# Kernel tuning notes

Hardware: AMD Instinct MI355X
Metric: run time of the kernel (lower is better)

The kernel has to match this reference:

```python
import jax, jax.numpy as jnp
import numpy as np

N_NODES = 50000
N_EDGES = 400000
IN_DIM = 4
HID = 32
NCLASSES = 4
N_ITERS = 3


def setup_inputs() -> dict:
    key = jax.random.key(0)
    ks = jax.random.split(key, 8)

    def w(k, shape, fan_in):
        return (jax.random.normal(k, shape, dtype=jnp.float32) / np.sqrt(fan_in)).astype(jnp.float32)

    x = jax.random.normal(ks[0], (3, N_NODES, IN_DIM), dtype=jnp.float32)
    edge_index = jax.random.randint(ks[1], (3, 2, N_EDGES), 0, N_NODES, dtype=jnp.int64)
    hi = HID + IN_DIM  # 36: feats of m = cat([H, X])
    return {
        "x": x,
        "edge_index": edge_index,
        "in_W": w(ks[2], (3, IN_DIM, HID), IN_DIM),
        "in_b": jnp.zeros((3, HID), jnp.float32),
        "eW1": w(ks[3], (3, 2 * hi, HID), 2 * hi),
        "eb1": jnp.zeros((3, HID), jnp.float32),
        "eW2": w(ks[4], (3, HID, 1), HID),
        "eb2": jnp.zeros((3, 1), jnp.float32),
        "nW1": w(ks[5], (3, 3 * hi, HID), 3 * hi),
        "nb1": jnp.zeros((3, HID), jnp.float32),
        "nW2": w(ks[6], (3, HID, HID), HID),
        "nb2": jnp.zeros((3, HID), jnp.float32),
    }


def _forward(x, edge_index, in_W, in_b, eW1, eb1, eW2, eb2, nW1, nb1, nW2, nb2):
    n_nodes = x.shape[1]

    def edge_net(j, m, row, col):
        # B: [E, C, 2*(h+in)] -- detached in the original module
        B = jax.lax.stop_gradient(jnp.concatenate([m[col], m[row]], axis=-1))
        t = jnp.tanh(B @ eW1[j] + eb1[j])
        t = jnp.tanh(t @ eW2[j] + eb2[j])  # [E, C, 1]
        return jax.nn.softmax(t, axis=1)  # softmax over class dim

    def node_net(j, m, ea, row, col):
        mi = jax.ops.segment_sum(ea * m[row], col, num_segments=n_nodes)
        mo = jax.ops.segment_sum(ea * m[col], row, num_segments=n_nodes)
        M = jnp.concatenate([mi, mo, m], axis=-1)  # [N, C, 3*(h+in)]
        t = jnp.tanh(M @ nW1[j] + nb1[j])
        return jnp.tanh(t @ nW2[j] + nb2[j])  # [N, C, hid]

    rows = [edge_index[j, 0] for j in range(3)]
    cols = [edge_index[j, 1] for j in range(3)]
    # X: node feats repeated per class, [N, C, in]
    X = [jnp.broadcast_to(x[j][:, None, :], (n_nodes, NCLASSES, x.shape[-1])) for j in range(3)]
    H = [jnp.tanh(X[j] @ in_W[j] + in_b[j]) for j in range(3)]
    m = [jnp.concatenate([H[j], X[j]], axis=-1) for j in range(3)]

    for _ in range(N_ITERS):
        for j in range(3):
            ea = edge_net(j, m[j], rows[j], cols[j])
            H[j] = node_net(j, m[j], ea, rows[j], cols[j])
        m = [jnp.concatenate([H[j], X[j]], axis=-1) for j in range(3)]

    # classify_node=False: final edge-network pass per plane, squeeze -> [E, C]
    ret = [edge_net(j, m[j], rows[j], cols[j])[..., 0] for j in range(3)]
    return jnp.concatenate(ret, axis=0)  # [3*E, C]


def reference(x, edge_index, in_W, in_b, eW1, eb1, eW2, eb2, nW1, nb1, nW2, nb2):
    return _forward(x, edge_index, in_W, in_b, eW1, eb1, eW2, eb2, nW1, nb1, nW2, nb2)
```

## Files before the change

### kernel.cpp

```cpp
#include <hip/hip_runtime.h>
#include <hip/hip_fp16.h>

#define N_NODES 50000
#define N_EDGES 400000
#define NCLS 4
#define HID 32
#define HI 36
#define ROWS_P (N_NODES * NCLS)
#define PADCAP 672000
#define SLICES 8
#define BUCKS_PER_SLICE (N_NODES / SLICES)

__device__ __forceinline__ float fast_tanh(float x) {
    x = fminf(15.0f, fmaxf(-15.0f, x));
    float e = __expf(2.0f * x);
    float d = 1.0f + e;
    float r = __builtin_amdgcn_rcpf(d);
    r = r * (2.0f - d * r);
    return 1.0f - 2.0f * r;
}

union F4H8 { float4 f4; __half2 h2[4]; };

__global__ void k_init(const float* __restrict__ x, const float* __restrict__ W,
                       const float* __restrict__ b, float* __restrict__ m) {
    unsigned t = blockIdx.x * 256 + threadIdx.x;
    if (t >= N_NODES * HI) return;
    unsigned idx = t % HI;
    unsigned n   = t / HI;
    float x0 = x[n * 4 + 0], x1 = x[n * 4 + 1];
    float x2 = x[n * 4 + 2], x3 = x[n * 4 + 3];
    float val;
    if (idx < 32) {
        float a = b[idx];
        a += x0 * W[idx] + x1 * W[32 + idx] + x2 * W[64 + idx] + x3 * W[96 + idx];
        val = fast_tanh(a);
    } else {
        val = (idx == 32) ? x0 : (idx == 33) ? x1 : (idx == 34) ? x2 : x3;
    }
    float* dst = m + (size_t)n * (NCLS * HI) + idx;
    dst[0] = val; dst[HI] = val; dst[2 * HI] = val; dst[3 * HI] = val;
}

__global__ void k_pass1(const int* __restrict__ rowI, const int* __restrict__ colI,
                        int* __restrict__ inCnt, int* __restrict__ outCnt,
                        int* __restrict__ tmpLi) {
    unsigned e = blockIdx.x * 256 + threadIdx.x;
    if (e >= N_EDGES) return;
    int r = rowI[e], cn = colI[e];
    int liIn  = atomicAdd(&inCnt[cn], 1);
    int liOut = atomicAdd(&outCnt[r], 1);
    tmpLi[e] = liIn | (liOut << 16);
}

__global__ void k_scan(const int* __restrict__ inCnt, const int* __restrict__ outCnt,
                       int* __restrict__ inOffRaw, int* __restrict__ pinOff,
                       int* __restrict__ poutOff) {
    const int* cnt = (blockIdx.x == 2) ? outCnt : inCnt;
    int* off = (blockIdx.x == 0) ? inOffRaw : (blockIdx.x == 1) ? pinOff : poutOff;
    bool pad = blockIdx.x != 0;
    __shared__ int sh[16];
    __shared__ int carry;
    int tid = threadIdx.x;
    int lane = tid & 63, wid = tid >> 6;
    if (tid == 0) carry = 0;
    __syncthreads();
    for (int base = 0; base < N_NODES; base += 1024) {
        int i = base + tid;
        int v = (i < N_NODES) ? cnt[i] : 0;
        if (pad) v = (v + 7) & ~7;
        int val = v;
#pragma unroll
        for (int d = 1; d < 64; d <<= 1) {
            int t = __shfl_up(val, d, 64);
            if (lane >= d) val += t;
        }
        if (lane == 63) sh[wid] = val;
        __syncthreads();
        if (tid < 16) {
            int s = sh[tid];
#pragma unroll
            for (int d = 1; d < 16; d <<= 1) {
                int t = __shfl_up(s, d, 16);
                if (tid >= d) s += t;
            }
            sh[tid] = s;
        }
        __syncthreads();
        int waveOff = (wid == 0) ? 0 : sh[wid - 1];
        int incl = val + waveOff + carry;
        if (i < N_NODES) off[i] = incl - v;
        __syncthreads();
        if (tid == 1023) carry = incl;
        __syncthreads();
    }
    if (tid == 0) off[N_NODES] = carry;
}

__global__ void k_pass2(const int* __restrict__ rowI, const int* __restrict__ colI,
                        const int* __restrict__ tmpLi,
                        const int* __restrict__ inOffRaw, const int* __restrict__ pinOff,
                        const int* __restrict__ poutOff,
                        int4* __restrict__ edgeRec,
                        unsigned short* __restrict__ inPrt,
                        unsigned short* __restrict__ outPrt) {
    unsigned b = blockIdx.x;
    unsigned slice = b & (SLICES - 1);
    unsigned e = (b >> 3) * 256 + threadIdx.x;
    if (e >= N_EDGES) return;
    int r = rowI[e], cn = colI[e];
    int li = tmpLi[e];
    int liIn  = li & 0xFFFF;
    int liOut = (int)(((unsigned)li) >> 16);
    unsigned lo = slice * BUCKS_PER_SLICE;
    if ((unsigned)(cn - lo) < BUCKS_PER_SLICE) {
        int dense = inOffRaw[cn] + liIn;
        int piP   = pinOff[cn] + liIn;
        int poP   = poutOff[r] + liOut;
        edgeRec[dense] = make_int4(r | (cn << 16), piP, poP, (int)e);
        inPrt[piP] = (unsigned short)r;
    }
    if ((unsigned)(r - lo) < BUCKS_PER_SLICE) {
        int poP = poutOff[r] + liOut;
        outPrt[poP] = (unsigned short)cn;
    }
}


__global__ void k_gemm5(const float* __restrict__ m,
                        const float* __restrict__ eW1, const float* __restrict__ nW1,
                        __half* __restrict__ u, __half* __restrict__ v,
                        __half* __restrict__ p, __half* __restrict__ q,
                        __half* __restrict__ r) {
    constexpr int RPB = 32;
    __shared__ float sm[RPB * HI];
    unsigned tid = threadIdx.x;
    unsigned r0  = blockIdx.x * RPB;
    {
        const float4* gsrc = reinterpret_cast<const float4*>(m + (size_t)r0 * HI);
        float4* ldst = reinterpret_cast<float4*>(sm);
        for (unsigned i = tid; i < RPB * HI / 4; i += 320) ldst[i] = gsrc[i];
    }
    unsigned o = tid % 160, grp = tid / 160;
    unsigned sub = o >> 5, oo = o & 31;
    const float* W = (sub == 0) ? eW1 : (sub == 1) ? eW1 + 36 * 32 :
                     (sub == 2) ? nW1 : (sub == 3) ? nW1 + 36 * 32 : nW1 + 72 * 32;
    __half* dsth   = (sub == 0) ? u : (sub == 1) ? v : (sub == 2) ? p :
                     (sub == 3) ? q : r;
    float wcol[36];
#pragma unroll
    for (int k = 0; k < 36; ++k) wcol[k] = W[k * 32 + oo];
    __syncthreads();
#pragma unroll
    for (int i = 0; i < 16; ++i) {
        unsigned rloc = grp * 16 + i;
        const float4* mv4 = reinterpret_cast<const float4*>(sm + rloc * HI);
        float acc = 0.f;
#pragma unroll
        for (int t = 0; t < 9; ++t) {
            float4 mv = mv4[t];
            acc += mv.x * wcol[4 * t + 0];
            acc += mv.y * wcol[4 * t + 1];
            acc += mv.z * wcol[4 * t + 2];
            acc += mv.w * wcol[4 * t + 3];
        }
        dsth[(size_t)(r0 + rloc) * 32 + oo] = __float2half_rn(acc);
    }
}

__global__ void k_gemm2(const float* __restrict__ m, const float* __restrict__ W0,
                        const float* __restrict__ W1,
                        __half* __restrict__ o0, __half* __restrict__ o1) {
    constexpr int RPB = 32;
    __shared__ float sm[RPB * HI];
    unsigned tid = threadIdx.x;
    unsigned r0  = blockIdx.x * RPB;
    {
        const float4* gsrc = reinterpret_cast<const float4*>(m + (size_t)r0 * HI);
        float4* ldst = reinterpret_cast<float4*>(sm);
        for (unsigned i = tid; i < RPB * HI / 4; i += 256) ldst[i] = gsrc[i];
    }
    unsigned o = tid % 64, grp = tid / 64;
    unsigned sub = o >> 5, oo = o & 31;
    const float* W = sub ? W1 : W0;
    __half* dst    = sub ? o1 : o0;
    float wcol[36];
#pragma unroll
    for (int k = 0; k < 36; ++k) wcol[k] = W[k * 32 + oo];
    __syncthreads();
#pragma unroll
    for (int i = 0; i < 8; ++i) {
        unsigned rloc = grp * 8 + i;
        const float4* mv4 = reinterpret_cast<const float4*>(sm + rloc * HI);
        float acc = 0.f;
#pragma unroll
        for (int t = 0; t < 9; ++t) {
            float4 mv = mv4[t];
            acc += mv.x * wcol[4 * t + 0];
            acc += mv.y * wcol[4 * t + 1];
            acc += mv.z * wcol[4 * t + 2];
            acc += mv.w * wcol[4 * t + 3];
        }
        dst[(size_t)(r0 + rloc) * 32 + oo] = __float2half_rn(acc);
    }
}

template <bool FINAL>
__global__ void k_edge(const int4* __restrict__ edgeRec,
                       const __half* __restrict__ u, const __half* __restrict__ v,
                       const float* __restrict__ b1, const float* __restrict__ w2,
                       const float* __restrict__ b2,
                       __half* __restrict__ eaIn, __half* __restrict__ eaOut,
                       float* __restrict__ dst) {
    unsigned g   = blockIdx.x * 256 + threadIdx.x;
    unsigned c   = g & 3;
    unsigned idx = g >> 2;
    int4 rec = edgeRec[idx];
    unsigned rc  = (unsigned)rec.x;
    unsigned row = rc & 0xFFFFu, col = rc >> 16;
    const float4* u4 = reinterpret_cast<const float4*>(u + (col * 4 + c) * 32);
    const float4* v4 = reinterpret_cast<const float4*>(v + (row * 4 + c) * 32);
    float t2 = b2[0];
#pragma unroll
    for (int i = 0; i < 4; ++i) {
        F4H8 U, V; U.f4 = u4[i]; V.f4 = v4[i];
#pragma unroll
        for (int jj = 0; jj < 4; ++jj) {
            float2 uf = __half22float2(U.h2[jj]);
            float2 vf = __half22float2(V.h2[jj]);
            int o = i * 8 + jj * 2;
            t2 += fast_tanh(uf.x + vf.x + b1[o])     * w2[o];
            t2 += fast_tanh(uf.y + vf.y + b1[o + 1]) * w2[o + 1];
        }
    }
    float s  = fast_tanh(t2);
    float m1 = fmaxf(s, __shfl_xor(s, 1, 4));
    float mx = fmaxf(m1, __shfl_xor(m1, 2, 4));
    float ex = __expf(s - mx);
    float sm = ex + __shfl_xor(ex, 1, 4);
    sm = sm + __shfl_xor(sm, 2, 4);
    float val = ex / sm;
    if (FINAL) {
        dst[(unsigned)rec.w * 4 + c] = val;
    } else {
        __half hv = __float2half_rn(val);
        eaIn[(size_t)c * PADCAP + (unsigned)rec.y] = hv;
        eaOut[(size_t)c * PADCAP + (unsigned)rec.z] = hv;
    }
}

__global__ void __launch_bounds__(64, 4)
k_node(float* __restrict__ m, const __half* __restrict__ rbuf,
       const __half* __restrict__ p, const __half* __restrict__ q,
       const __half* __restrict__ eaInT, const __half* __restrict__ eaOutT,
       const int* __restrict__ pinOff, const int* __restrict__ poutOff,
       const unsigned short* __restrict__ inPrt,
       const unsigned short* __restrict__ outPrt,
       const float* __restrict__ nb1,
       const float* __restrict__ nW2, const float* __restrict__ nb2) {
    unsigned lane = threadIdx.x;
    unsigned c2 = lane >> 5, k = lane & 31;
    unsigned n = blockIdx.x;
    unsigned gOff0 = c2 * 32 + k;
    unsigned gOff1 = gOff0 + 64;

    float b1k = nb1[k];
    float h0 = __half2float(rbuf[((size_t)n * 4 + c2) * 32 + k]) + b1k;
    float h1 = __half2float(rbuf[((size_t)n * 4 + c2 + 2) * 32 + k]) + b1k;

    int bi0 = pinOff[n],  biE = pinOff[n + 1];
    int bo0 = poutOff[n], boE = poutOff[n + 1];
    __builtin_assume((bi0 & 7) == 0);
    __builtin_assume((bo0 & 7) == 0);

    auto accum = [&](const __half* __restrict__ base, uint4 prtv, uint4 e0v, uint4 e1v) {
        unsigned pr0 = prtv.x & 0xFFFFu, pr1 = prtv.x >> 16;
        unsigned pr2 = prtv.y & 0xFFFFu, pr3 = prtv.y >> 16;
        unsigned pr4 = prtv.z & 0xFFFFu, pr5 = prtv.z >> 16;
        unsigned pr6 = prtv.w & 0xFFFFu, pr7 = prtv.w >> 16;
        __half g0h[8], g1h[8];
        const __half* r0p = base + (size_t)pr0 * 128u; g0h[0] = r0p[gOff0]; g1h[0] = r0p[gOff1];
        const __half* r1p = base + (size_t)pr1 * 128u; g0h[1] = r1p[gOff0]; g1h[1] = r1p[gOff1];
        const __half* r2p = base + (size_t)pr2 * 128u; g0h[2] = r2p[gOff0]; g1h[2] = r2p[gOff1];
        const __half* r3p = base + (size_t)pr3 * 128u; g0h[3] = r3p[gOff0]; g1h[3] = r3p[gOff1];
        const __half* r4p = base + (size_t)pr4 * 128u; g0h[4] = r4p[gOff0]; g1h[4] = r4p[gOff1];
        const __half* r5p = base + (size_t)pr5 * 128u; g0h[5] = r5p[gOff0]; g1h[5] = r5p[gOff1];
        const __half* r6p = base + (size_t)pr6 * 128u; g0h[6] = r6p[gOff0]; g1h[6] = r6p[gOff1];
        const __half* r7p = base + (size_t)pr7 * 128u; g0h[7] = r7p[gOff0]; g1h[7] = r7p[gOff1];
        union { uint4 u4; __half2 h2[4]; } E0, E1;
        E0.u4 = e0v; E1.u4 = e1v;
#pragma unroll
        for (int ii = 0; ii < 4; ++ii) {
            float2 A0 = __half22float2(E0.h2[ii]);
            float2 A1 = __half22float2(E1.h2[ii]);
            h0 += A0.x * __half2float(g0h[2 * ii]) + A0.y * __half2float(g0h[2 * ii + 1]);
            h1 += A1.x * __half2float(g1h[2 * ii]) + A1.y * __half2float(g1h[2 * ii + 1]);
        }
    };

    uint4 oprt = {0, 0, 0, 0}, oe0 = {0, 0, 0, 0}, oe1 = {0, 0, 0, 0};
    if (bo0 < boE) {
        oprt = *(const uint4*)(outPrt + bo0);
        oe0  = *(const uint4*)(eaOutT + (size_t)c2 * PADCAP + bo0);
        oe1  = *(const uint4*)(eaOutT + (size_t)(c2 + 2) * PADCAP + bo0);
    }

    if (bi0 < biE) {
        uint4 cprt = *(const uint4*)(inPrt + bi0);
        uint4 ce0  = *(const uint4*)(eaInT + (size_t)c2 * PADCAP + bi0);
        uint4 ce1  = *(const uint4*)(eaInT + (size_t)(c2 + 2) * PADCAP + bi0);
        for (int b = bi0; b < biE; b += 8) {
            uint4 nprt = cprt, ne0 = ce0, ne1 = ce1;
            if (b + 8 < biE) {
                nprt = *(const uint4*)(inPrt + b + 8);
                ne0  = *(const uint4*)(eaInT + (size_t)c2 * PADCAP + b + 8);
                ne1  = *(const uint4*)(eaInT + (size_t)(c2 + 2) * PADCAP + b + 8);
            }
            accum(p, cprt, ce0, ce1);
            cprt = nprt; ce0 = ne0; ce1 = ne1;
        }
    }
    if (bo0 < boE) {
        uint4 cprt = oprt, ce0 = oe0, ce1 = oe1;
        for (int b = bo0; b < boE; b += 8) {
            uint4 nprt = cprt, ne0 = ce0, ne1 = ce1;
            if (b + 8 < boE) {
                nprt = *(const uint4*)(outPrt + b + 8);
                ne0  = *(const uint4*)(eaOutT + (size_t)c2 * PADCAP + b + 8);
                ne1  = *(const uint4*)(eaOutT + (size_t)(c2 + 2) * PADCAP + b + 8);
            }
            accum(q, cprt, ce0, ce1);
            cprt = nprt; ce0 = ne0; ce1 = ne1;
        }
    }

    float t0 = fast_tanh(h0);
    float t1 = fast_tanh(h1);
    float hh0 = nb2[k], hh1 = hh0;
#pragma unroll
    for (int kk = 0; kk < 32; ++kk) {
        float w = nW2[kk * 32 + k];
        float s0 = __shfl(t0, (int)(c2 * 32 + kk), 64);
        float s1 = __shfl(t1, (int)(c2 * 32 + kk), 64);
        hh0 += s0 * w;
        hh1 += s1 * w;
    }
    m[((size_t)n * 4 + c2) * HI + k]     = fast_tanh(hh0);
    m[((size_t)n * 4 + c2 + 2) * HI + k] = fast_tanh(hh1);
}

extern "C" void kernel_launch(void* const* d_in, const int* in_sizes, int n_in,
                              void* d_out, int out_size, void* d_ws, size_t ws_size,
                              hipStream_t stream) {
    const float* x   = (const float*)d_in[0];
    const int*   ei  = (const int*)d_in[1];
    const float* inW = (const float*)d_in[2];
    const float* inb = (const float*)d_in[3];
    const float* eW1 = (const float*)d_in[4];
    const float* eb1 = (const float*)d_in[5];
    const float* eW2 = (const float*)d_in[6];
    const float* eb2 = (const float*)d_in[7];
    const float* nW1 = (const float*)d_in[8];
    const float* nb1 = (const float*)d_in[9];
    const float* nW2 = (const float*)d_in[10];
    const float* nb2 = (const float*)d_in[11];
    float* out = (float*)d_out;

    float*  m     = (float*)d_ws;
    __half* u     = (__half*)(m + (size_t)ROWS_P * HI);
    __half* v     = u + (size_t)ROWS_P * 32;
    __half* p     = v + (size_t)ROWS_P * 32;
    __half* q     = p + (size_t)ROWS_P * 32;
    __half* rbuf  = q + (size_t)ROWS_P * 32;
    __half* eaIn  = rbuf + (size_t)ROWS_P * 32;
    __half* eaOut = eaIn + (size_t)PADCAP * 4;
    unsigned short* inPrt  = (unsigned short*)(eaOut + (size_t)PADCAP * 4);
    unsigned short* outPrt = inPrt + PADCAP;
    int4*   edgeRec = (int4*)(outPrt + PADCAP);
    int*    inOffRaw = (int*)(edgeRec + N_EDGES);
    int*    pinOff   = inOffRaw + (N_NODES + 1);
    int*    poutOff  = pinOff + (N_NODES + 1);
    int*    inCnt    = poutOff + (N_NODES + 1);
    int*    outCnt   = inCnt + N_NODES;
    int*    tmpLi    = (int*)u;

    const int gridE = (N_EDGES + 255) / 256;
    const size_t zeroBytes = (size_t)PADCAP * 4 * 2 * 2 + (size_t)PADCAP * 2 * 2;

    for (int j = 0; j < 3; ++j) {
        const int*   rowI = ei + (size_t)j * 2 * N_EDGES;
        const int*   colI = rowI + N_EDGES;
        const float* eW1j = eW1 + j * 72 * 32;
        const float* eb1j = eb1 + j * 32;
        const float* eW2j = eW2 + j * 32;
        const float* eb2j = eb2 + j;
        const float* nW1j = nW1 + j * 108 * 32;
        const float* nb1j = nb1 + j * 32;
        const float* nW2j = nW2 + j * 1024;
        const float* nb2j = nb2 + j * 32;

        hipMemsetAsync(inCnt, 0, 2 * N_NODES * sizeof(int), stream);
        hipMemsetAsync(eaIn, 0, zeroBytes, stream);
        k_pass1<<<gridE, 256, 0, stream>>>(rowI, colI, inCnt, outCnt, tmpLi);
        k_scan<<<3, 1024, 0, stream>>>(inCnt, outCnt, inOffRaw, pinOff, poutOff);
        k_pass2<<<gridE * SLICES, 256, 0, stream>>>(rowI, colI, tmpLi,
                                                    inOffRaw, pinOff, poutOff,
                                                    edgeRec, inPrt, outPrt);

        k_init<<<(N_NODES * HI + 255) / 256, 256, 0, stream>>>(
            x + (size_t)j * N_NODES * 4, inW + j * 128, inb + j * 32, m);

        for (int it = 0; it < 3; ++it) {
            k_gemm5<<<ROWS_P / 32, 320, 0, stream>>>(m, eW1j, nW1j, u, v, p, q, rbuf);
            k_edge<false><<<N_EDGES * 4 / 256, 256, 0, stream>>>(
                edgeRec, u, v, eb1j, eW2j, eb2j, eaIn, eaOut, nullptr);
            k_node<<<N_NODES, 64, 0, stream>>>(m, rbuf, p, q, eaIn, eaOut,
                                               pinOff, poutOff, inPrt, outPrt,
                                               nb1j, nW2j, nb2j);
        }
        k_gemm2<<<ROWS_P / 32, 256, 0, stream>>>(m, eW1j, eW1j + 36 * 32, u, v);
        k_edge<true><<<N_EDGES * 4 / 256, 256, 0, stream>>>(
            edgeRec, u, v, eb1j, eW2j, eb2j, nullptr, nullptr,
            out + (size_t)j * N_EDGES * 4);
    }
}
```

Before: 1.703 ms.

## Fold biases into GEMMs, use fdot2, cheaper tanh, two nodes per block

Several changes at once. The edge and node first-layer biases are folded into the gemm5/gemm2 accumulators, so k_edge and k_node no longer add them per element. tanh becomes a bare exp2 plus rcp with no clamp and no Newton step. k_edge adds u+v in half precision, k_node accumulates with fdot2, and k_node packs two nodes per 128-thread block with different launch bounds. These cut ALU work and launch granularity, at the cost of some precision (half add, unrefined rcp, half products in fdot2).

```diff
diff --git a/kernel.cpp b/kernel.cpp
--- a/kernel.cpp
+++ b/kernel.cpp
@@ -12,13 +12,23 @@
 #define BUCKS_PER_SLICE (N_NODES / SLICES)
 
 __device__ __forceinline__ float fast_tanh(float x) {
-    x = fminf(15.0f, fmaxf(-15.0f, x));
-    float e = __expf(2.0f * x);
-    float d = 1.0f + e;
-    float r = __builtin_amdgcn_rcpf(d);
-    r = r * (2.0f - d * r);
-    return 1.0f - 2.0f * r;
-}
+    float e = __builtin_amdgcn_exp2f(x * 2.885390081777927f);
+    float r = __builtin_amdgcn_rcpf(1.0f + e);
+    return fmaf(-2.0f, r, 1.0f);
+}
+
+#if __has_builtin(__builtin_amdgcn_fdot2)
+typedef _Float16 h2v __attribute__((ext_vector_type(2)));
+__device__ __forceinline__ float fdot2f(__half2 a, __half2 b, float c) {
+    return __builtin_amdgcn_fdot2(__builtin_bit_cast(h2v, a),
+                                  __builtin_bit_cast(h2v, b), c, false);
+}
+#else
+__device__ __forceinline__ float fdot2f(__half2 a, __half2 b, float c) {
+    float2 af = __half22float2(a), bf = __half22float2(b);
+    return c + af.x * bf.x + af.y * bf.y;
+}
+#endif
 
 union F4H8 { float4 f4; __half2 h2[4]; };
 
@@ -129,6 +139,7 @@
 
 __global__ void k_gemm5(const float* __restrict__ m,
                         const float* __restrict__ eW1, const float* __restrict__ nW1,
+                        const float* __restrict__ eb1, const float* __restrict__ nb1,
                         __half* __restrict__ u, __half* __restrict__ v,
                         __half* __restrict__ p, __half* __restrict__ q,
                         __half* __restrict__ r) {
@@ -147,6 +158,7 @@
                      (sub == 2) ? nW1 : (sub == 3) ? nW1 + 36 * 32 : nW1 + 72 * 32;
     __half* dsth   = (sub == 0) ? u : (sub == 1) ? v : (sub == 2) ? p :
                      (sub == 3) ? q : r;
+    float bias = (sub == 0) ? eb1[oo] : (sub == 4) ? nb1[oo] : 0.f;
     float wcol[36];
 #pragma unroll
     for (int k = 0; k < 36; ++k) wcol[k] = W[k * 32 + oo];
@@ -155,7 +167,7 @@
     for (int i = 0; i < 16; ++i) {
         unsigned rloc = grp * 16 + i;
         const float4* mv4 = reinterpret_cast<const float4*>(sm + rloc * HI);
-        float acc = 0.f;
+        float acc = bias;
 #pragma unroll
         for (int t = 0; t < 9; ++t) {
             float4 mv = mv4[t];
@@ -169,7 +181,7 @@
 }
 
 __global__ void k_gemm2(const float* __restrict__ m, const float* __restrict__ W0,
-                        const float* __restrict__ W1,
+                        const float* __restrict__ W1, const float* __restrict__ eb1,
                         __half* __restrict__ o0, __half* __restrict__ o1) {
     constexpr int RPB = 32;
     __shared__ float sm[RPB * HI];
@@ -184,6 +196,7 @@
     unsigned sub = o >> 5, oo = o & 31;
     const float* W = sub ? W1 : W0;
     __half* dst    = sub ? o1 : o0;
+    float bias = sub ? 0.f : eb1[oo];
     float wcol[36];
 #pragma unroll
     for (int k = 0; k < 36; ++k) wcol[k] = W[k * 32 + oo];
@@ -192,7 +205,7 @@
     for (int i = 0; i < 8; ++i) {
         unsigned rloc = grp * 8 + i;
         const float4* mv4 = reinterpret_cast<const float4*>(sm + rloc * HI);
-        float acc = 0.f;
+        float acc = bias;
 #pragma unroll
         for (int t = 0; t < 9; ++t) {
             float4 mv = mv4[t];
@@ -208,8 +221,7 @@
 template <bool FINAL>
 __global__ void k_edge(const int4* __restrict__ edgeRec,
                        const __half* __restrict__ u, const __half* __restrict__ v,
-                       const float* __restrict__ b1, const float* __restrict__ w2,
-                       const float* __restrict__ b2,
+                       const float* __restrict__ w2, const float* __restrict__ b2,
                        __half* __restrict__ eaIn, __half* __restrict__ eaOut,
                        float* __restrict__ dst) {
     unsigned g   = blockIdx.x * 256 + threadIdx.x;
@@ -226,11 +238,10 @@
         F4H8 U, V; U.f4 = u4[i]; V.f4 = v4[i];
 #pragma unroll
         for (int jj = 0; jj < 4; ++jj) {
-            float2 uf = __half22float2(U.h2[jj]);
-            float2 vf = __half22float2(V.h2[jj]);
+            float2 sf = __half22float2(__hadd2(U.h2[jj], V.h2[jj]));
             int o = i * 8 + jj * 2;
-            t2 += fast_tanh(uf.x + vf.x + b1[o])     * w2[o];
-            t2 += fast_tanh(uf.y + vf.y + b1[o + 1]) * w2[o + 1];
+            t2 += fast_tanh(sf.x) * w2[o];
+            t2 += fast_tanh(sf.y) * w2[o + 1];
         }
     }
     float s  = fast_tanh(t2);
@@ -249,24 +260,23 @@
     }
 }
 
-__global__ void __launch_bounds__(64, 4)
+__global__ void __launch_bounds__(128, 8)
 k_node(float* __restrict__ m, const __half* __restrict__ rbuf,
        const __half* __restrict__ p, const __half* __restrict__ q,
        const __half* __restrict__ eaInT, const __half* __restrict__ eaOutT,
        const int* __restrict__ pinOff, const int* __restrict__ poutOff,
        const unsigned short* __restrict__ inPrt,
        const unsigned short* __restrict__ outPrt,
-       const float* __restrict__ nb1,
        const float* __restrict__ nW2, const float* __restrict__ nb2) {
-    unsigned lane = threadIdx.x;
+    unsigned lane = threadIdx.x & 63;
+    unsigned wv   = threadIdx.x >> 6;
     unsigned c2 = lane >> 5, k = lane & 31;
-    unsigned n = blockIdx.x;
+    unsigned n = blockIdx.x * 2 + wv;
     unsigned gOff0 = c2 * 32 + k;
     unsigned gOff1 = gOff0 + 64;
 
-    float b1k = nb1[k];
-    float h0 = __half2float(rbuf[((size_t)n * 4 + c2) * 32 + k]) + b1k;
-    float h1 = __half2float(rbuf[((size_t)n * 4 + c2 + 2) * 32 + k]) + b1k;
+    float h0 = __half2float(rbuf[((size_t)n * 4 + c2) * 32 + k]);
+    float h1 = __half2float(rbuf[((size_t)n * 4 + c2 + 2) * 32 + k]);
 
     int bi0 = pinOff[n],  biE = pinOff[n + 1];
     int bo0 = poutOff[n], boE = poutOff[n + 1];
@@ -291,10 +301,8 @@
         E0.u4 = e0v; E1.u4 = e1v;
 #pragma unroll
         for (int ii = 0; ii < 4; ++ii) {
-            float2 A0 = __half22float2(E0.h2[ii]);
-            float2 A1 = __half22float2(E1.h2[ii]);
-            h0 += A0.x * __half2float(g0h[2 * ii]) + A0.y * __half2float(g0h[2 * ii + 1]);
-            h1 += A1.x * __half2float(g1h[2 * ii]) + A1.y * __half2float(g1h[2 * ii + 1]);
+            h0 = fdot2f(E0.h2[ii], __halves2half2(g0h[2 * ii], g0h[2 * ii + 1]), h0);
+            h1 = fdot2f(E1.h2[ii], __halves2half2(g1h[2 * ii], g1h[2 * ii + 1]), h1);
         }
     };
 
@@ -411,16 +419,17 @@
             x + (size_t)j * N_NODES * 4, inW + j * 128, inb + j * 32, m);
 
         for (int it = 0; it < 3; ++it) {
-            k_gemm5<<<ROWS_P / 32, 320, 0, stream>>>(m, eW1j, nW1j, u, v, p, q, rbuf);
+            k_gemm5<<<ROWS_P / 32, 320, 0, stream>>>(m, eW1j, nW1j, eb1j, nb1j,
+                                                     u, v, p, q, rbuf);
             k_edge<false><<<N_EDGES * 4 / 256, 256, 0, stream>>>(
-                edgeRec, u, v, eb1j, eW2j, eb2j, eaIn, eaOut, nullptr);
-            k_node<<<N_NODES, 64, 0, stream>>>(m, rbuf, p, q, eaIn, eaOut,
-                                               pinOff, poutOff, inPrt, outPrt,
-                                               nb1j, nW2j, nb2j);
-        }
-        k_gemm2<<<ROWS_P / 32, 256, 0, stream>>>(m, eW1j, eW1j + 36 * 32, u, v);
+                edgeRec, u, v, eW2j, eb2j, eaIn, eaOut, nullptr);
+            k_node<<<N_NODES / 2, 128, 0, stream>>>(m, rbuf, p, q, eaIn, eaOut,
+                                                    pinOff, poutOff, inPrt, outPrt,
+                                                    nW2j, nb2j);
+        }
+        k_gemm2<<<ROWS_P / 32, 256, 0, stream>>>(m, eW1j, eW1j + 36 * 32, eb1j, u, v);
         k_edge<true><<<N_EDGES * 4 / 256, 256, 0, stream>>>(
-            edgeRec, u, v, eb1j, eW2j, eb2j, nullptr, nullptr,
+            edgeRec, u, v, eW2j, eb2j, nullptr, nullptr,
             out + (size_t)j * N_EDGES * 4);
     }
 }
```

After: 2.050 ms. 1.2x slower.
